# Performance work log

Measured on AMD Instinct MI355X. Metric: run time of the kernel, lower is better.

## Reference

```python
import jax, jax.numpy as jnp
import numpy as np


def setup_inputs() -> dict:
    key = jax.random.key(0)
    ks = jax.random.split(key, 7)
    B, T, I, H, O = 256, 1024, 3, 128, 3
    s = 1.0 / np.sqrt(H)  # torch nn.RNN/Linear default init scale
    return {
        "inputs": jax.random.normal(ks[0], (B, T, I), dtype=jnp.float32),
        "W_ih": jax.random.uniform(ks[1], (H, I), jnp.float32, -s, s),
        "W_hh": jax.random.uniform(ks[2], (H, H), jnp.float32, -s, s),
        "b_ih": jax.random.uniform(ks[3], (H,), jnp.float32, -s, s),
        "b_hh": jax.random.uniform(ks[4], (H,), jnp.float32, -s, s),
        "h0": jnp.zeros((1, H), dtype=jnp.float32),  # learned initial hidden (init zeros)
        "W_out": jax.random.uniform(ks[5], (O, H), jnp.float32, -s, s),
        "b_out": jax.random.uniform(ks[6], (O,), jnp.float32, -s, s),
    }


def reference(inputs, W_ih, W_hh, b_ih, b_hh, h0, W_out, b_out):
    # inputs: [B, T, I]; Elman RNN with tanh, batch_first, single layer.
    B = inputs.shape[0]
    # Precompute input projection for all timesteps: [T, B, H]
    x_proj = jnp.einsum('bti,hi->tbh', inputs, W_ih) + b_ih + b_hh
    h_init = jnp.broadcast_to(h0, (B, h0.shape[1]))

    def step(h, xp):
        h_new = jnp.tanh(xp + h @ W_hh.T)
        return h_new, h_new

    _, hiddens_tbh = jax.lax.scan(step, h_init, x_proj)
    hiddens = jnp.transpose(hiddens_tbh, (1, 0, 2))  # [B, T, H]
    output = jnp.einsum('bth,oh->bto', hiddens, W_out) + b_out  # [B, T, O]
    return output, hiddens
```

## Files before the change

### kernel.cpp

```cpp
#include <hip/hip_runtime.h>

#define BB 256
#define TT 1024
#define II 3
#define HH 128
#define OO 3
#define NT 576

#if __has_builtin(__builtin_amdgcn_exp2f)
#define EXP2F __builtin_amdgcn_exp2f
#else
#define EXP2F exp2f
#endif
#if __has_builtin(__builtin_amdgcn_rcpf)
#define RCPF __builtin_amdgcn_rcpf
#else
#define RCPF(x) (1.0f / (x))
#endif

__device__ __forceinline__ float fast_tanh(float x) {
    float e = EXP2F(x * 2.885390081777927f);
    return 1.0f - 2.0f * RCPF(e + 1.0f);
}

__device__ __forceinline__ void bar_lds() {
    asm volatile("s_waitcnt lgkmcnt(0)\n\ts_barrier" ::: "memory");
}

__global__ __launch_bounds__(NT) void rnn_kernel(
    const float* __restrict__ x,
    const float* __restrict__ Wih,
    const float* __restrict__ Whh,
    const float* __restrict__ bih,
    const float* __restrict__ bhh,
    const float* __restrict__ h0,
    const float* __restrict__ Wout,
    const float* __restrict__ bout,
    float* __restrict__ out,
    float* __restrict__ hid)
{
    __shared__ __align__(16) float4 xs[TT];
    __shared__ __align__(16) float hbuf[2][HH];

    const int tid = threadIdx.x;
    const int b = blockIdx.x;

    const float* xb = x + (size_t)b * TT * II;
    for (int idx = tid; idx < TT * II; idx += NT) {
        int t = idx / 3;
        int c = idx - t * 3;
        ((float*)&xs[t])[c] = xb[idx];
    }
    if (tid < HH) hbuf[0][tid] = h0[tid];

    if (tid < 512) {
        const int lane = tid & 63;
        const int wv   = tid >> 6;
        const int o16  = lane & 15;
        const int sub  = lane >> 4;
        const int h    = wv * 16 + o16;

        float w[32];
        {
            const float4* wp = (const float4*)(Whh + h * HH + 32 * sub);
#pragma unroll
            for (int j = 0; j < 8; j++) {
                float4 v = wp[j];
                w[4 * j + 0] = v.x;
                w[4 * j + 1] = v.y;
                w[4 * j + 2] = v.z;
                w[4 * j + 3] = v.w;
            }
        }
        const float wi0 = Wih[h * II + 0];
        const float wi1 = Wih[h * II + 1];
        const float wi2 = Wih[h * II + 2];
        const float bias = bih[h] + bhh[h];

        bar_lds();

        for (int t = 0; t < TT; t++) {
            const float* hcur = hbuf[t & 1];
            float* hnext = hbuf[(t + 1) & 1];

            float a0 = 0.f, a1 = 0.f, a2 = 0.f, a3 = 0.f;
            if (sub == 0) {
                float4 xv = xs[t];
                a0 = fmaf(xv.x, wi0, bias);
                a0 = fmaf(xv.y, wi1, a0);
                a0 = fmaf(xv.z, wi2, a0);
            }
            const float4* hv = (const float4*)(hcur + 32 * sub);
#pragma unroll
            for (int j = 0; j < 8; j++) {
                float4 hh = hv[j];
                a0 = fmaf(w[4 * j + 0], hh.x, a0);
                a1 = fmaf(w[4 * j + 1], hh.y, a1);
                a2 = fmaf(w[4 * j + 2], hh.z, a2);
                a3 = fmaf(w[4 * j + 3], hh.w, a3);
            }
            float s = (a0 + a1) + (a2 + a3);
            s += __shfl_xor(s, 16);
            s += __shfl_xor(s, 32);
            float th = fast_tanh(s);
            if (sub == 0) hnext[h] = th;
            bar_lds();
        }
    } else {
        const int L = tid - 512;
        const float w00 = Wout[0 * HH + 2 * L], w01 = Wout[0 * HH + 2 * L + 1];
        const float w10 = Wout[1 * HH + 2 * L], w11 = Wout[1 * HH + 2 * L + 1];
        const float w20 = Wout[2 * HH + 2 * L], w21 = Wout[2 * HH + 2 * L + 1];
        const float b0 = bout[0], b1 = bout[1], b2 = bout[2];
        float* ob = out + (size_t)b * TT * OO;
        float* hb = hid + (size_t)b * TT * HH;

        bar_lds();

        for (int t = 0; t < TT; t++) {
            if (t > 0) {
                const float2 hv = ((const float2*)hbuf[t & 1])[L];
                ((float2*)(hb + (size_t)(t - 1) * HH))[L] = hv;
                float p0 = fmaf(hv.x, w00, hv.y * w01);
                float p1 = fmaf(hv.x, w10, hv.y * w11);
                float p2 = fmaf(hv.x, w20, hv.y * w21);
#pragma unroll
                for (int m = 32; m >= 1; m >>= 1) {
                    p0 += __shfl_xor(p0, m);
                    p1 += __shfl_xor(p1, m);
                    p2 += __shfl_xor(p2, m);
                }
                if (L == 0) {
                    float* o = ob + (size_t)(t - 1) * OO;
                    o[0] = p0 + b0;
                    o[1] = p1 + b1;
                    o[2] = p2 + b2;
                }
            }
            bar_lds();
        }
        {
            const float2 hv = ((const float2*)hbuf[0])[L];
            ((float2*)(hb + (size_t)(TT - 1) * HH))[L] = hv;
            float p0 = fmaf(hv.x, w00, hv.y * w01);
            float p1 = fmaf(hv.x, w10, hv.y * w11);
            float p2 = fmaf(hv.x, w20, hv.y * w21);
#pragma unroll
            for (int m = 32; m >= 1; m >>= 1) {
                p0 += __shfl_xor(p0, m);
                p1 += __shfl_xor(p1, m);
                p2 += __shfl_xor(p2, m);
            }
            if (L == 0) {
                float* o = ob + (size_t)(TT - 1) * OO;
                o[0] = p0 + b0;
                o[1] = p1 + b1;
                o[2] = p2 + b2;
            }
        }
    }
}

extern "C" void kernel_launch(void* const* d_in, const int* in_sizes, int n_in,
                              void* d_out, int out_size, void* d_ws, size_t ws_size,
                              hipStream_t stream) {
    const float* x    = (const float*)d_in[0];
    const float* Wih  = (const float*)d_in[1];
    const float* Whh  = (const float*)d_in[2];
    const float* bih  = (const float*)d_in[3];
    const float* bhh  = (const float*)d_in[4];
    const float* h0   = (const float*)d_in[5];
    const float* Wout = (const float*)d_in[6];
    const float* bout = (const float*)d_in[7];

    float* out = (float*)d_out;
    float* hid = out + (size_t)BB * TT * OO;

    rnn_kernel<<<BB, NT, 0, stream>>>(x, Wih, Whh, bih, bhh, h0, Wout, bout, out, hid);
}
```

Before: 542.6 us.

## Split recurrence across 4 waves with 64-wide rows and DPP/permlane reductions

```diff
diff --git a/kernel.cpp b/kernel.cpp
--- a/kernel.cpp
+++ b/kernel.cpp
@@ -5,7 +5,7 @@
 #define II 3
 #define HH 128
 #define OO 3
-#define NT 576
+#define NT 320
 
 #if __has_builtin(__builtin_amdgcn_exp2f)
 #define EXP2F __builtin_amdgcn_exp2f
@@ -25,6 +25,20 @@
 
 __device__ __forceinline__ void bar_lds() {
     asm volatile("s_waitcnt lgkmcnt(0)\n\ts_barrier" ::: "memory");
+}
+
+__device__ __forceinline__ float xor32_sum(float s) {
+    float a = s, b = s;
+    asm("v_permlane32_swap_b32 %0, %1" : "+&v"(a), "+&v"(b));
+    return a + b;
+}
+
+__device__ __forceinline__ float quad_reduce(float p) {
+    p += __uint_as_float(__builtin_amdgcn_update_dpp(
+        0, (int)__float_as_uint(p), 0xB1, 0xF, 0xF, true));
+    p += __uint_as_float(__builtin_amdgcn_update_dpp(
+        0, (int)__float_as_uint(p), 0x4E, 0xF, 0xF, true));
+    return p;
 }
 
 __global__ __launch_bounds__(NT) void rnn_kernel(
@@ -41,6 +55,7 @@
 {
     __shared__ __align__(16) float4 xs[TT];
     __shared__ __align__(16) float hbuf[2][HH];
+    __shared__ __align__(16) float psum[2][OO * 16];
 
     const int tid = threadIdx.x;
     const int b = blockIdx.x;
@@ -53,23 +68,20 @@
     }
     if (tid < HH) hbuf[0][tid] = h0[tid];
 
-    if (tid < 512) {
+    if (tid < 256) {
         const int lane = tid & 63;
         const int wv   = tid >> 6;
-        const int o16  = lane & 15;
-        const int sub  = lane >> 4;
-        const int h    = wv * 16 + o16;
-
-        float w[32];
+        const int o32  = lane & 31;
+        const int sub  = lane >> 5;
+        const int h    = wv * 32 + o32;
+
+        float w[64];
         {
-            const float4* wp = (const float4*)(Whh + h * HH + 32 * sub);
+            const float4* wrow = (const float4*)(Whh + h * HH);
 #pragma unroll
-            for (int j = 0; j < 8; j++) {
-                float4 v = wp[j];
-                w[4 * j + 0] = v.x;
-                w[4 * j + 1] = v.y;
-                w[4 * j + 2] = v.z;
-                w[4 * j + 3] = v.w;
+            for (int j = 0; j < 16; j++) {
+                float4 v = wrow[2 * j + sub];
+                w[4*j+0] = v.x; w[4*j+1] = v.y; w[4*j+2] = v.z; w[4*j+3] = v.w;
             }
         }
         const float wi0 = Wih[h * II + 0];
@@ -77,12 +89,14 @@
         const float wi2 = Wih[h * II + 2];
         const float bias = bih[h] + bhh[h];
 
+        const float4* hr0 = (const float4*)hbuf[0] + sub;
+        const float4* hr1 = (const float4*)hbuf[1] + sub;
+        float* hw0 = &hbuf[1][h];
+        float* hw1 = &hbuf[0][h];
+
         bar_lds();
 
-        for (int t = 0; t < TT; t++) {
-            const float* hcur = hbuf[t & 1];
-            float* hnext = hbuf[(t + 1) & 1];
-
+        auto cstep = [&](int t, const float4* hr, float* hw) {
             float a0 = 0.f, a1 = 0.f, a2 = 0.f, a3 = 0.f;
             if (sub == 0) {
                 float4 xv = xs[t];
@@ -90,72 +104,100 @@
                 a0 = fmaf(xv.y, wi1, a0);
                 a0 = fmaf(xv.z, wi2, a0);
             }
-            const float4* hv = (const float4*)(hcur + 32 * sub);
 #pragma unroll
-            for (int j = 0; j < 8; j++) {
-                float4 hh = hv[j];
-                a0 = fmaf(w[4 * j + 0], hh.x, a0);
-                a1 = fmaf(w[4 * j + 1], hh.y, a1);
-                a2 = fmaf(w[4 * j + 2], hh.z, a2);
-                a3 = fmaf(w[4 * j + 3], hh.w, a3);
-            }
-            float s = (a0 + a1) + (a2 + a3);
-            s += __shfl_xor(s, 16);
-            s += __shfl_xor(s, 32);
+            for (int j = 0; j < 16; j++) {
+                float4 hh = hr[2 * j];
+                a0 = fmaf(w[4*j+0], hh.x, a0);
+                a1 = fmaf(w[4*j+1], hh.y, a1);
+                a2 = fmaf(w[4*j+2], hh.z, a2);
+                a3 = fmaf(w[4*j+3], hh.w, a3);
+            }
+            float s = xor32_sum((a0 + a1) + (a2 + a3));
             float th = fast_tanh(s);
-            if (sub == 0) hnext[h] = th;
+            if (sub == 0) *hw = th;
             bar_lds();
+        };
+
+        for (int t = 0; t < TT; t += 2) {
+            cstep(t, hr0, hw0);
+            cstep(t + 1, hr1, hw1);
         }
     } else {
-        const int L = tid - 512;
+        const int L = tid - 256;
         const float w00 = Wout[0 * HH + 2 * L], w01 = Wout[0 * HH + 2 * L + 1];
         const float w10 = Wout[1 * HH + 2 * L], w11 = Wout[1 * HH + 2 * L + 1];
         const float w20 = Wout[2 * HH + 2 * L], w21 = Wout[2 * HH + 2 * L + 1];
-        const float b0 = bout[0], b1 = bout[1], b2 = bout[2];
+        const float bL = (L == 0) ? bout[0] : (L == 1) ? bout[1]
+                       : (L == 2) ? bout[2] : 0.f;
         float* ob = out + (size_t)b * TT * OO;
         float* hb = hid + (size_t)b * TT * HH;
+        const int q = L >> 2;
+        const bool qlead = (L & 3) == 0;
 
         bar_lds();
 
-        for (int t = 0; t < TT; t++) {
-            if (t > 0) {
-                const float2 hv = ((const float2*)hbuf[t & 1])[L];
+        auto sstep = [&](int t, const float* hcur, float* psA, const float* psB) {
+            if (t >= 1) {
+                const float2 hv = ((const float2*)hcur)[L];
                 ((float2*)(hb + (size_t)(t - 1) * HH))[L] = hv;
                 float p0 = fmaf(hv.x, w00, hv.y * w01);
                 float p1 = fmaf(hv.x, w10, hv.y * w11);
                 float p2 = fmaf(hv.x, w20, hv.y * w21);
-#pragma unroll
-                for (int m = 32; m >= 1; m >>= 1) {
-                    p0 += __shfl_xor(p0, m);
-                    p1 += __shfl_xor(p1, m);
-                    p2 += __shfl_xor(p2, m);
+                p0 = quad_reduce(p0);
+                p1 = quad_reduce(p1);
+                p2 = quad_reduce(p2);
+                if (qlead) {
+                    psA[0 * 16 + q] = p0;
+                    psA[1 * 16 + q] = p1;
+                    psA[2 * 16 + q] = p2;
                 }
-                if (L == 0) {
-                    float* o = ob + (size_t)(t - 1) * OO;
-                    o[0] = p0 + b0;
-                    o[1] = p1 + b1;
-                    o[2] = p2 + b2;
-                }
+            }
+            if (t >= 2 && L < OO) {
+                const float4* pp = (const float4*)(psB + L * 16);
+                float4 u0 = pp[0], u1 = pp[1], u2 = pp[2], u3 = pp[3];
+                float s0 = ((u0.x + u0.y) + (u0.z + u0.w)) +
+                           ((u1.x + u1.y) + (u1.z + u1.w));
+                float s1 = ((u2.x + u2.y) + (u2.z + u2.w)) +
+                           ((u3.x + u3.y) + (u3.z + u3.w));
+                ob[(size_t)(t - 2) * OO + L] = s0 + s1 + bL;
             }
             bar_lds();
-        }
+        };
+
+        for (int t = 0; t < TT; t += 2) {
+            sstep(t, hbuf[0], psum[0], psum[1]);
+            sstep(t + 1, hbuf[1], psum[1], psum[0]);
+        }
+
         {
             const float2 hv = ((const float2*)hbuf[0])[L];
             ((float2*)(hb + (size_t)(TT - 1) * HH))[L] = hv;
             float p0 = fmaf(hv.x, w00, hv.y * w01);
             float p1 = fmaf(hv.x, w10, hv.y * w11);
             float p2 = fmaf(hv.x, w20, hv.y * w21);
-#pragma unroll
-            for (int m = 32; m >= 1; m >>= 1) {
-                p0 += __shfl_xor(p0, m);
-                p1 += __shfl_xor(p1, m);
-                p2 += __shfl_xor(p2, m);
-            }
-            if (L == 0) {
-                float* o = ob + (size_t)(TT - 1) * OO;
-                o[0] = p0 + b0;
-                o[1] = p1 + b1;
-                o[2] = p2 + b2;
+            p0 = quad_reduce(p0);
+            p1 = quad_reduce(p1);
+            p2 = quad_reduce(p2);
+            if (qlead) {
+                psum[0][0 * 16 + q] = p0;
+                psum[0][1 * 16 + q] = p1;
+                psum[0][2 * 16 + q] = p2;
+            }
+            if (L < OO) {
+                const float4* pp = (const float4*)(psum[1] + L * 16);
+                float4 u0 = pp[0], u1 = pp[1], u2 = pp[2], u3 = pp[3];
+                float s0 = ((u0.x + u0.y) + (u0.z + u0.w)) +
+                           ((u1.x + u1.y) + (u1.z + u1.w));
+                float s1 = ((u2.x + u2.y) + (u2.z + u2.w)) +
+                           ((u3.x + u3.y) + (u3.z + u3.w));
+                ob[(size_t)(TT - 2) * OO + L] = s0 + s1 + bL;
+                const float4* pq = (const float4*)(psum[0] + L * 16);
+                float4 v0 = pq[0], v1 = pq[1], v2 = pq[2], v3 = pq[3];
+                float r0 = ((v0.x + v0.y) + (v0.z + v0.w)) +
+                           ((v1.x + v1.y) + (v1.z + v1.w));
+                float r1 = ((v2.x + v2.y) + (v2.z + v2.w)) +
+                           ((v3.x + v3.y) + (v3.z + v3.w));
+                ob[(size_t)(TT - 1) * OO + L] = r0 + r1 + bL;
             }
         }
     }
```

After: 625.3 us. 1.15x slower.

## Run each sequence's recurrence in a single wavefront with register-resident W_hh

Applied to the files above, without the earlier changes.

```diff
diff --git a/kernel.cpp b/kernel.cpp
--- a/kernel.cpp
+++ b/kernel.cpp
@@ -5,7 +5,7 @@
 #define II 3
 #define HH 128
 #define OO 3
-#define NT 576
+#define NT 64
 
 #if __has_builtin(__builtin_amdgcn_exp2f)
 #define EXP2F __builtin_amdgcn_exp2f
@@ -18,16 +18,32 @@
 #define RCPF(x) (1.0f / (x))
 #endif
 
+typedef __attribute__((ext_vector_type(2))) float f2;
+
 __device__ __forceinline__ float fast_tanh(float x) {
     float e = EXP2F(x * 2.885390081777927f);
     return 1.0f - 2.0f * RCPF(e + 1.0f);
 }
 
-__device__ __forceinline__ void bar_lds() {
-    asm volatile("s_waitcnt lgkmcnt(0)\n\ts_barrier" ::: "memory");
+__device__ __forceinline__ f2 pk_fma(f2 a, f2 b, f2 c) {
+    f2 d;
+    asm("v_pk_fma_f32 %0, %1, %2, %3" : "=v"(d) : "v"(a), "v"(b), "v"(c));
+    return d;
 }
 
-__global__ __launch_bounds__(NT) void rnn_kernel(
+__device__ __forceinline__ void lds_order() { asm volatile("" ::: "memory"); }
+
+template <int CTRL>
+__device__ __forceinline__ float dpp_add(float p) {
+    return p + __uint_as_float(__builtin_amdgcn_update_dpp(
+        0, (int)__float_as_uint(p), CTRL, 0xF, 0xF, true));
+}
+#define DPP_XOR1 0xB1
+#define DPP_XOR2 0x4E
+#define DPP_HMIR 0x141
+#define DPP_MIRR 0x140
+
+__global__ __launch_bounds__(NT, 1) void rnn_kernel(
     const float* __restrict__ x,
     const float* __restrict__ Wih,
     const float* __restrict__ Whh,
@@ -40,124 +56,116 @@
     float* __restrict__ hid)
 {
     __shared__ __align__(16) float4 xs[TT];
-    __shared__ __align__(16) float hbuf[2][HH];
+    __shared__ __align__(16) float hbuf[HH];
+    __shared__ __align__(16) float psum[2][12];
 
-    const int tid = threadIdx.x;
+    const int lane = threadIdx.x;
     const int b = blockIdx.x;
 
-    const float* xb = x + (size_t)b * TT * II;
-    for (int idx = tid; idx < TT * II; idx += NT) {
-        int t = idx / 3;
-        int c = idx - t * 3;
-        ((float*)&xs[t])[c] = xb[idx];
+    {
+        const float* xb = x + (size_t)b * TT * II;
+        const float4* xb4 = (const float4*)xb + lane * 12;
+        float v[48];
+#pragma unroll
+        for (int j = 0; j < 12; ++j) {
+            float4 q = xb4[j];
+            v[4 * j + 0] = q.x; v[4 * j + 1] = q.y;
+            v[4 * j + 2] = q.z; v[4 * j + 3] = q.w;
+        }
+#pragma unroll
+        for (int tt = 0; tt < 16; ++tt)
+            xs[lane * 16 + tt] =
+                float4{v[3 * tt], v[3 * tt + 1], v[3 * tt + 2], 0.f};
     }
-    if (tid < HH) hbuf[0][tid] = h0[tid];
+    ((float2*)hbuf)[lane] = ((const float2*)h0)[lane];
+    lds_order();
 
-    if (tid < 512) {
-        const int lane = tid & 63;
-        const int wv   = tid >> 6;
-        const int o16  = lane & 15;
-        const int sub  = lane >> 4;
-        const int h    = wv * 16 + o16;
+    f2 w0[64], w1[64];
+    {
+        const float4* r0 = (const float4*)(Whh + (size_t)(2 * lane) * HH);
+        const float4* r1 = (const float4*)(Whh + (size_t)(2 * lane + 1) * HH);
+#pragma unroll
+        for (int c = 0; c < 32; ++c) {
+            float4 a = r0[c];
+            w0[2 * c]     = f2{a.x, a.y};
+            w0[2 * c + 1] = f2{a.z, a.w};
+            float4 q = r1[c];
+            w1[2 * c]     = f2{q.x, q.y};
+            w1[2 * c + 1] = f2{q.z, q.w};
+        }
+    }
+    const int r0i = 2 * lane, r1i = 2 * lane + 1;
+    const float wi00 = Wih[r0i * II + 0], wi01 = Wih[r0i * II + 1], wi02 = Wih[r0i * II + 2];
+    const float wi10 = Wih[r1i * II + 0], wi11 = Wih[r1i * II + 1], wi12 = Wih[r1i * II + 2];
+    const float bias0 = bih[r0i] + bhh[r0i];
+    const float bias1 = bih[r1i] + bhh[r1i];
+    const float wo00 = Wout[0 * HH + 2 * lane], wo01 = Wout[0 * HH + 2 * lane + 1];
+    const float wo10 = Wout[1 * HH + 2 * lane], wo11 = Wout[1 * HH + 2 * lane + 1];
+    const float wo20 = Wout[2 * HH + 2 * lane], wo21 = Wout[2 * HH + 2 * lane + 1];
+    const float boL = (lane < OO) ? bout[lane] : 0.f;
 
-        float w[32];
-        {
-            const float4* wp = (const float4*)(Whh + h * HH + 32 * sub);
+    float2* hb2 = (float2*)(hid + (size_t)b * TT * HH);
+    float* ob = out + (size_t)b * TT * OO;
+    const float4* hb4 = (const float4*)hbuf;
+    const int o = lane & 15;
+
+    for (int t = 0; t < TT; ++t) {
+        const int par = t & 1;
+        if (t > 0 && lane < OO) {
+            const float* pp = psum[par ^ 1];
+            float4 g4 = *(const float4*)(pp + lane * 4);
+            ob[(size_t)(t - 1) * OO + lane] =
+                ((g4.x + g4.y) + (g4.z + g4.w)) + boL;
+        }
+        float4 xv = xs[t];
+        f2 a0[4] = {f2{0.f, 0.f}, f2{0.f, 0.f}, f2{0.f, 0.f}, f2{0.f, 0.f}};
+        f2 a1[4] = {f2{0.f, 0.f}, f2{0.f, 0.f}, f2{0.f, 0.f}, f2{0.f, 0.f}};
 #pragma unroll
-            for (int j = 0; j < 8; j++) {
-                float4 v = wp[j];
-                w[4 * j + 0] = v.x;
-                w[4 * j + 1] = v.y;
-                w[4 * j + 2] = v.z;
-                w[4 * j + 3] = v.w;
+        for (int gq = 0; gq < 4; ++gq) {
+            float4 hcg[8];
+#pragma unroll
+            for (int j = 0; j < 8; ++j) hcg[j] = hb4[gq * 8 + j];
+#pragma unroll
+            for (int j = 0; j < 8; ++j) {
+                const int c = gq * 8 + j;
+                f2 hh0 = f2{hcg[j].x, hcg[j].y};
+                f2 hh1 = f2{hcg[j].z, hcg[j].w};
+                a0[c & 3] = pk_fma(w0[2 * c],     hh0, a0[c & 3]);
+                a0[c & 3] = pk_fma(w0[2 * c + 1], hh1, a0[c & 3]);
+                a1[c & 3] = pk_fma(w1[2 * c],     hh0, a1[c & 3]);
+                a1[c & 3] = pk_fma(w1[2 * c + 1], hh1, a1[c & 3]);
             }
         }
-        const float wi0 = Wih[h * II + 0];
-        const float wi1 = Wih[h * II + 1];
-        const float wi2 = Wih[h * II + 2];
-        const float bias = bih[h] + bhh[h];
-
-        bar_lds();
-
-        for (int t = 0; t < TT; t++) {
-            const float* hcur = hbuf[t & 1];
-            float* hnext = hbuf[(t + 1) & 1];
-
-            float a0 = 0.f, a1 = 0.f, a2 = 0.f, a3 = 0.f;
-            if (sub == 0) {
-                float4 xv = xs[t];
-                a0 = fmaf(xv.x, wi0, bias);
-                a0 = fmaf(xv.y, wi1, a0);
-                a0 = fmaf(xv.z, wi2, a0);
-            }
-            const float4* hv = (const float4*)(hcur + 32 * sub);
-#pragma unroll
-            for (int j = 0; j < 8; j++) {
-                float4 hh = hv[j];
-                a0 = fmaf(w[4 * j + 0], hh.x, a0);
-                a1 = fmaf(w[4 * j + 1], hh.y, a1);
-                a2 = fmaf(w[4 * j + 2], hh.z, a2);
-                a3 = fmaf(w[4 * j + 3], hh.w, a3);
-            }
-            float s = (a0 + a1) + (a2 + a3);
-            s += __shfl_xor(s, 16);
-            s += __shfl_xor(s, 32);
-            float th = fast_tanh(s);
-            if (sub == 0) hnext[h] = th;
-            bar_lds();
+        f2 s0v = (a0[0] + a0[1]) + (a0[2] + a0[3]);
+        f2 s1v = (a1[0] + a1[1]) + (a1[2] + a1[3]);
+        float xp0 = fmaf(xv.z, wi02, fmaf(xv.y, wi01, fmaf(xv.x, wi00, bias0)));
+        float xp1 = fmaf(xv.z, wi12, fmaf(xv.y, wi11, fmaf(xv.x, wi10, bias1)));
+        float val0 = fast_tanh((s0v.x + s0v.y) + xp0);
+        float val1 = fast_tanh((s1v.x + s1v.y) + xp1);
+        float2 hv = float2{val0, val1};
+        ((float2*)hbuf)[lane] = hv;
+        lds_order();
+        hb2[(size_t)t * 64 + lane] = hv;
+        float p0 = fmaf(wo01, val1, wo00 * val0);
+        float p1 = fmaf(wo11, val1, wo10 * val0);
+        float p2 = fmaf(wo21, val1, wo20 * val0);
+        p0 = dpp_add<DPP_XOR1>(p0); p0 = dpp_add<DPP_XOR2>(p0);
+        p0 = dpp_add<DPP_HMIR>(p0); p0 = dpp_add<DPP_MIRR>(p0);
+        p1 = dpp_add<DPP_XOR1>(p1); p1 = dpp_add<DPP_XOR2>(p1);
+        p1 = dpp_add<DPP_HMIR>(p1); p1 = dpp_add<DPP_MIRR>(p1);
+        p2 = dpp_add<DPP_XOR1>(p2); p2 = dpp_add<DPP_XOR2>(p2);
+        p2 = dpp_add<DPP_HMIR>(p2); p2 = dpp_add<DPP_MIRR>(p2);
+        if (o < OO) {
+            float pv = (o == 0) ? p0 : (o == 1) ? p1 : p2;
+            psum[par][o * 4 + (lane >> 4)] = pv;
         }
-    } else {
-        const int L = tid - 512;
-        const float w00 = Wout[0 * HH + 2 * L], w01 = Wout[0 * HH + 2 * L + 1];
-        const float w10 = Wout[1 * HH + 2 * L], w11 = Wout[1 * HH + 2 * L + 1];
-        const float w20 = Wout[2 * HH + 2 * L], w21 = Wout[2 * HH + 2 * L + 1];
-        const float b0 = bout[0], b1 = bout[1], b2 = bout[2];
-        float* ob = out + (size_t)b * TT * OO;
-        float* hb = hid + (size_t)b * TT * HH;
-
-        bar_lds();
-
-        for (int t = 0; t < TT; t++) {
-            if (t > 0) {
-                const float2 hv = ((const float2*)hbuf[t & 1])[L];
-                ((float2*)(hb + (size_t)(t - 1) * HH))[L] = hv;
-                float p0 = fmaf(hv.x, w00, hv.y * w01);
-                float p1 = fmaf(hv.x, w10, hv.y * w11);
-                float p2 = fmaf(hv.x, w20, hv.y * w21);
-#pragma unroll
-                for (int m = 32; m >= 1; m >>= 1) {
-                    p0 += __shfl_xor(p0, m);
-                    p1 += __shfl_xor(p1, m);
-                    p2 += __shfl_xor(p2, m);
-                }
-                if (L == 0) {
-                    float* o = ob + (size_t)(t - 1) * OO;
-                    o[0] = p0 + b0;
-                    o[1] = p1 + b1;
-                    o[2] = p2 + b2;
-                }
-            }
-            bar_lds();
-        }
-        {
-            const float2 hv = ((const float2*)hbuf[0])[L];
-            ((float2*)(hb + (size_t)(TT - 1) * HH))[L] = hv;
-            float p0 = fmaf(hv.x, w00, hv.y * w01);
-            float p1 = fmaf(hv.x, w10, hv.y * w11);
-            float p2 = fmaf(hv.x, w20, hv.y * w21);
-#pragma unroll
-            for (int m = 32; m >= 1; m >>= 1) {
-                p0 += __shfl_xor(p0, m);
-                p1 += __shfl_xor(p1, m);
-                p2 += __shfl_xor(p2, m);
-            }
-            if (L == 0) {
-                float* o = ob + (size_t)(TT - 1) * OO;
-                o[0] = p0 + b0;
-                o[1] = p1 + b1;
-                o[2] = p2 + b2;
-            }
-        }
+        lds_order();
+    }
+    if (lane < OO) {
+        const float* pp = psum[(TT - 1) & 1];
+        float4 g4 = *(const float4*)(pp + lane * 4);
+        ob[(size_t)(TT - 1) * OO + lane] =
+            ((g4.x + g4.y) + (g4.z + g4.w)) + boL;
     }
 }
 
```

After: 1.610 ms. +196.8%, slower.
